# Kernel optimization log

Measured on AMD Instinct MI355X. Metric: run time of the kernel, lower is better.

The kernel has to match this reference:

```python
import jax, jax.numpy as jnp
import numpy as np

B, S, H = 4, 2048, 1024
NH, HD = 16, 64  # num heads, head size

def setup_inputs() -> dict:
    key = jax.random.key(0)
    ks = jax.random.split(key, 7)
    s = 1.0 / np.sqrt(H)
    return {
        "hidden_states": jax.random.normal(ks[0], (B, S, H), dtype=jnp.float32),
        "Wq": jax.random.normal(ks[1], (H, H), dtype=jnp.float32) * s,
        "bq": jax.random.normal(ks[2], (H,), dtype=jnp.float32) * 0.02,
        "Wk": jax.random.normal(ks[3], (H, H), dtype=jnp.float32) * s,
        "bk": jax.random.normal(ks[4], (H,), dtype=jnp.float32) * 0.02,
        "Wv": jax.random.normal(ks[5], (H, H), dtype=jnp.float32) * s,
        "bv": jax.random.normal(ks[6], (H,), dtype=jnp.float32) * 0.02,
    }

def _split_heads(x):
    # [B,S,H] -> [B,NH,S,HD]
    return x.reshape(B, S, NH, HD).transpose(0, 2, 1, 3)

def reference(hidden_states, Wq, bq, Wk, bk, Wv, bv):
    q = _split_heads(hidden_states @ Wq + bq)
    k = _split_heads(hidden_states @ Wk + bk)
    v = _split_heads(hidden_states @ Wv + bv)
    scores = jnp.einsum('bhqd,bhkd->bhqk', q, k) / np.sqrt(HD).astype(np.float32)
    probs = jax.nn.softmax(scores, axis=-1)  # dropout p=0 (eval)
    ctx = jnp.einsum('bhqk,bhkd->bhqd', probs, v)
    # [B,NH,S,HD] -> [B,S,H]
    return ctx.transpose(0, 2, 1, 3).reshape(B, S, H)
```

## Files before the change

### kernel.cpp

```cpp
#include <hip/hip_runtime.h>


typedef __bf16 bf16x8 __attribute__((ext_vector_type(8)));
typedef __bf16 bf16x4 __attribute__((ext_vector_type(4)));
typedef float f32x4 __attribute__((ext_vector_type(4)));
typedef unsigned short ushort8 __attribute__((ext_vector_type(8)));

#define MFMA16(a, b, c) __builtin_amdgcn_mfma_f32_16x16x32_bf16(a, b, c, 0, 0, 0)

static __device__ __forceinline__ unsigned short f2bf(float x) {
    unsigned int u = __float_as_uint(x);
    u = u + 0x7fffu + ((u >> 16) & 1u);
    return (unsigned short)(u >> 16);
}

static __device__ __forceinline__ void gload_lds16(const void* g, void* l) {
    __builtin_amdgcn_global_load_lds(
        (const __attribute__((address_space(1))) unsigned int*)g,
        (__attribute__((address_space(3))) unsigned int*)l,
        16, 0, 0);
}

__global__ void convert_x(const float* __restrict__ x, unsigned short* __restrict__ y) {
    size_t i = ((size_t)blockIdx.x * 256 + threadIdx.x) * 8;
    float4 a = *(const float4*)(x + i);
    float4 b = *(const float4*)(x + i + 4);
    ushort8 o;
    o[0] = f2bf(a.x); o[1] = f2bf(a.y); o[2] = f2bf(a.z); o[3] = f2bf(a.w);
    o[4] = f2bf(b.x); o[5] = f2bf(b.y); o[6] = f2bf(b.z); o[7] = f2bf(b.w);
    *(ushort8*)(y + i) = o;
}

__global__ void wtrans(const float* __restrict__ Wq, const float* __restrict__ Wk,
                       const float* __restrict__ Wv, unsigned short* __restrict__ Wt) {
    __shared__ float T[64][68];
    const float* W = blockIdx.z == 0 ? Wq : (blockIdx.z == 1 ? Wk : Wv);
    int k0 = blockIdx.y * 64, n0 = blockIdx.x * 64;
    int t = threadIdx.x;
    int rr = t >> 2, c4 = (t & 3) * 16;
    for (int j = 0; j < 16; j += 4) {
        float4 v = *(const float4*)(W + (size_t)(k0 + rr) * 1024 + n0 + c4 + j);
        T[rr][c4 + j] = v.x; T[rr][c4 + j + 1] = v.y;
        T[rr][c4 + j + 2] = v.z; T[rr][c4 + j + 3] = v.w;
    }
    __syncthreads();
    unsigned short* o = Wt + ((size_t)blockIdx.z << 20) + (size_t)(n0 + rr) * 1024 + k0 + c4;
    for (int j = 0; j < 16; j += 8) {
        ushort8 v;
        for (int u = 0; u < 8; u++) v[u] = f2bf(T[c4 + j + u][rr]);
        *(ushort8*)(o + j) = v;
    }
}

__global__ __launch_bounds__(256, 2) void qkv_gemm(
    const unsigned short* __restrict__ Xb, const unsigned short* __restrict__ Wt,
    const float* __restrict__ bq, const float* __restrict__ bk, const float* __restrict__ bv,
    unsigned short* __restrict__ Q, unsigned short* __restrict__ K,
    unsigned short* __restrict__ Vt) {
    __shared__ __align__(16) unsigned char smem[65536];

    int tid = threadIdx.x;
    int wave = tid >> 6, lane = tid & 63;
    int g = lane >> 4, r = lane & 15;
    int f = blockIdx.x + blockIdx.y * 24;
    int nf = (f & 7) * 192 + (f >> 3);
    int bx = nf % 24, by = nf / 24;
    int m0 = by * 128;
    int col0 = bx * 128;
    int qkv = col0 >> 10;
    int ncol0 = col0 & 1023;
    int wr = wave >> 1, wc = wave & 1;
    const unsigned short* Wb = Wt + ((size_t)qkv << 20);

    auto stage = [&](int buf, int k0) {
#pragma unroll
        for (int i = 0; i < 4; i++) {
            int slot = (i * 4 + wave) * 64 + lane;
            int row = slot >> 3;
            int ch = (slot & 7) ^ (row & 7);
            gload_lds16(Xb + (size_t)(m0 + row) * 1024 + k0 + ch * 8,
                        smem + buf * 16384 + (i * 4 + wave) * 1024);
            gload_lds16(Wb + (size_t)(ncol0 + row) * 1024 + k0 + ch * 8,
                        smem + 32768 + buf * 16384 + (i * 4 + wave) * 1024);
        }
    };

    f32x4 acc[4][4];
    for (int m = 0; m < 4; m++)
        for (int n = 0; n < 4; n++)
            for (int u = 0; u < 4; u++) acc[m][n][u] = 0.f;

    stage(0, 0);
    __syncthreads();
    int buf = 0;
    for (int t = 0; t < 16; ++t) {
        if (t < 15) stage(buf ^ 1, (t + 1) * 64);
        const unsigned char* Ab = smem + buf * 16384;
        const unsigned char* Bb = smem + 32768 + buf * 16384;
#pragma unroll
        for (int kk = 0; kk < 2; kk++) {
            bf16x8 af[4], bfv[4];
#pragma unroll
            for (int m = 0; m < 4; m++) {
                int row = wr * 64 + m * 16 + r;
                af[m] = *(const bf16x8*)(Ab + row * 128 + ((((kk * 4 + g) << 4)) ^ ((row & 7) << 4)));
            }
#pragma unroll
            for (int n = 0; n < 4; n++) {
                int row = wc * 64 + n * 16 + r;
                bfv[n] = *(const bf16x8*)(Bb + row * 128 + ((((kk * 4 + g) << 4)) ^ ((row & 7) << 4)));
            }
#pragma unroll
            for (int m = 0; m < 4; m++)
#pragma unroll
                for (int n = 0; n < 4; n++)
                    acc[m][n] = MFMA16(af[m], bfv[n], acc[m][n]);
        }
        __syncthreads();
        buf ^= 1;
    }

    if (qkv != 2) {
        const float* bias = (qkv == 0) ? bq : bk;
        unsigned short* dst = (qkv == 0) ? Q : K;
        float scale = (qkv == 0) ? 0.18033688011112042f : 1.0f;
        for (int m = 0; m < 4; m++)
            for (int n = 0; n < 4; n++) {
                int C = ncol0 + wc * 64 + n * 16 + r;
                int h = C >> 6, d = C & 63;
                float bb = bias[C];
                for (int reg = 0; reg < 4; reg++) {
                    int R = m0 + wr * 64 + m * 16 + 4 * g + reg;
                    int b = R >> 11, s = R & 2047;
                    float val = (acc[m][n][reg] + bb) * scale;
                    dst[((((size_t)b * 16 + h) * 2048) + s) * 64 + d] = f2bf(val);
                }
            }
    } else {
        unsigned short* T = (unsigned short*)smem;
        for (int m = 0; m < 4; m++)
            for (int n = 0; n < 4; n++) {
                int Cl = wc * 64 + n * 16 + r;
                float bb = bv[ncol0 + Cl];
                for (int reg = 0; reg < 4; reg++) {
                    int Rl = wr * 64 + m * 16 + 4 * g + reg;
                    T[Rl * 136 + Cl] = f2bf(acc[m][n][reg] + bb);
                }
            }
        __syncthreads();
        int dl = tid >> 1, s0c = (tid & 1) * 64;
        int Cg = ncol0 + dl;
        int h = Cg >> 6, dd = Cg & 63;
        int bidx = m0 >> 11;
        int sbase = (m0 & 2047) + s0c;
        unsigned short* dstp = Vt + (((size_t)bidx * 16 + h) * 64 + dd) * 2048 + sbase;
        for (int jc = 0; jc < 8; jc++) {
            ushort8 v;
            for (int u = 0; u < 8; u++) v[u] = T[(s0c + jc * 8 + u) * 136 + dl];
            *(ushort8*)(dstp + jc * 8) = v;
        }
    }
}

__global__ __launch_bounds__(256, 4) void attn(
    const unsigned short* __restrict__ Q, const unsigned short* __restrict__ K,
    const unsigned short* __restrict__ Vt, float* __restrict__ out) {
    __shared__ __align__(16) unsigned char lds[40960];

    int tid = threadIdx.x, w = tid >> 6, lane = tid & 63;
    int r = lane & 15, g = lane >> 4;
    int f = blockIdx.x + (blockIdx.y << 4);
    int nf = ((f & 7) << 7) | (f >> 3);
    int qt = nf & 15, bh = nf >> 4;
    int q0 = qt * 128 + w * 32;
    const unsigned short* Qb = Q + (size_t)bh * 2048 * 64;
    const unsigned short* Kb = K + (size_t)bh * 2048 * 64;
    const unsigned short* Vb = Vt + (size_t)bh * 64 * 2048;

    auto stageKV = [&](int buf, int kv0) {
#pragma unroll
        for (int i = 0; i < 2; i++) {
            int slot = (i * 4 + w) * 64 + lane;
            int row = slot >> 3;
            int ch = (slot & 7) ^ (row & 7);
            gload_lds16(Kb + (size_t)(kv0 + row) * 64 + ch * 8,
                        lds + buf * 8192 + (i * 4 + w) * 1024);
            gload_lds16(Vb + (size_t)row * 2048 + kv0 + ch * 8,
                        lds + 16384 + buf * 8192 + (i * 4 + w) * 1024);
        }
    };

    bf16x8 qf[2][2];
#pragma unroll
    for (int qi = 0; qi < 2; qi++)
#pragma unroll
        for (int sl = 0; sl < 2; sl++)
            qf[qi][sl] = *(const bf16x8*)(Qb + (size_t)(q0 + qi * 16 + r) * 64 + sl * 32 + g * 8);

    bf16x8 ones8;
#pragma unroll
    for (int i = 0; i < 8; i++) ones8[i] = (__bf16)1.0f;

    f32x4 o[2][4], ls[2];
#pragma unroll
    for (int qi = 0; qi < 2; qi++) {
#pragma unroll
        for (int u = 0; u < 4; u++) ls[qi][u] = 0.f;
#pragma unroll
        for (int d = 0; d < 4; d++)
#pragma unroll
            for (int u = 0; u < 4; u++) o[qi][d][u] = 0.f;
    }

    stageKV(0, 0);
    __syncthreads();
    int buf = 0;
    int rsw = (r & 7) << 4;
    unsigned char* Pw = lds + 32768 + w * 2048;

    for (int t = 0; t < 32; ++t) {
        if (t < 31) stageKV(buf ^ 1, (t + 1) * 64);
        const unsigned char* Kl = lds + buf * 8192;
        const unsigned char* Vl = lds + 16384 + buf * 8192;

        f32x4 s[2][4];
#pragma unroll
        for (int qi = 0; qi < 2; qi++)
#pragma unroll
            for (int kvt = 0; kvt < 4; kvt++)
#pragma unroll
                for (int u = 0; u < 4; u++) s[qi][kvt][u] = 0.f;
#pragma unroll
        for (int kvt = 0; kvt < 4; kvt++) {
            const unsigned char* kp = Kl + (kvt * 16 + r) * 128;
            bf16x8 k0 = *(const bf16x8*)(kp + ((g << 4) ^ rsw));
            bf16x8 k1 = *(const bf16x8*)(kp + (((4 + g) << 4) ^ rsw));
            s[0][kvt] = MFMA16(k0, qf[0][0], s[0][kvt]);
            s[0][kvt] = MFMA16(k1, qf[0][1], s[0][kvt]);
            s[1][kvt] = MFMA16(k0, qf[1][0], s[1][kvt]);
            s[1][kvt] = MFMA16(k1, qf[1][1], s[1][kvt]);
        }

#pragma unroll
        for (int qi = 0; qi < 2; qi++) {
#pragma unroll
            for (int kvt = 0; kvt < 4; kvt++) {
                bf16x4 pw;
                pw[0] = (__bf16)__builtin_amdgcn_exp2f(s[qi][kvt][0]);
                pw[1] = (__bf16)__builtin_amdgcn_exp2f(s[qi][kvt][1]);
                pw[2] = (__bf16)__builtin_amdgcn_exp2f(s[qi][kvt][2]);
                pw[3] = (__bf16)__builtin_amdgcn_exp2f(s[qi][kvt][3]);
                *(bf16x4*)(Pw + (r << 7) + ((kvt * 32 + g * 8) ^ rsw)) = pw;
            }
#pragma unroll
            for (int ks2 = 0; ks2 < 2; ks2++) {
                bf16x8 pf = *(const bf16x8*)(Pw + (r << 7) + ((ks2 * 64 + g * 16) ^ rsw));
                ls[qi] = MFMA16(ones8, pf, ls[qi]);
#pragma unroll
                for (int d = 0; d < 4; d++) {
                    bf16x8 vf = *(const bf16x8*)(Vl + (d * 16 + r) * 128 + (((ks2 * 4 + g) << 4) ^ rsw));
                    o[qi][d] = MFMA16(vf, pf, o[qi][d]);
                }
            }
        }

        __syncthreads();
        buf ^= 1;
    }

    int b = bh >> 4, h = bh & 15;
#pragma unroll
    for (int qi = 0; qi < 2; qi++) {
        float inv = 1.0f / ls[qi][0];
        float* ob = out + ((size_t)b * 2048 + q0 + qi * 16 + r) * 1024 + h * 64;
#pragma unroll
        for (int d = 0; d < 4; d++) {
            float4 v;
            v.x = o[qi][d][0] * inv; v.y = o[qi][d][1] * inv;
            v.z = o[qi][d][2] * inv; v.w = o[qi][d][3] * inv;
            *(float4*)(ob + d * 16 + 4 * g) = v;
        }
    }
}

extern "C" void kernel_launch(void* const* d_in, const int* in_sizes, int n_in,
                              void* d_out, int out_size, void* d_ws, size_t ws_size,
                              hipStream_t stream) {
    const float* X  = (const float*)d_in[0];
    const float* Wq = (const float*)d_in[1];
    const float* bq = (const float*)d_in[2];
    const float* Wk = (const float*)d_in[3];
    const float* bk = (const float*)d_in[4];
    const float* Wv = (const float*)d_in[5];
    const float* bv = (const float*)d_in[6];
    float* out = (float*)d_out;
    char* ws = (char*)d_ws;

    unsigned short* Xb  = (unsigned short*)(ws);
    unsigned short* Wt  = (unsigned short*)(ws + 16777216);
    unsigned short* Qw  = (unsigned short*)(ws + 23068672);
    unsigned short* Kw  = (unsigned short*)(ws + 39845888);
    unsigned short* Vtw = (unsigned short*)(ws + 56623104);

    hipLaunchKernelGGL(convert_x, dim3(4096), dim3(256), 0, stream, X, Xb);
    hipLaunchKernelGGL(wtrans, dim3(16, 16, 3), dim3(256), 0, stream, Wq, Wk, Wv, Wt);
    hipLaunchKernelGGL(qkv_gemm, dim3(24, 64), dim3(256), 0, stream,
                       Xb, Wt, bq, bk, bv, Qw, Kw, Vtw);
    hipLaunchKernelGGL(attn, dim3(16, 64), dim3(256), 0, stream, Qw, Kw, Vtw, out);
}
```

Baseline: 157.0 us.

## Software-pipeline attention loop: overlap next QK with previous softmax-PV using triple-buffered V

```diff
diff --git a/kernel.cpp b/kernel.cpp
--- a/kernel.cpp
+++ b/kernel.cpp
@@ -162,10 +162,10 @@
     }
 }
 
-__global__ __launch_bounds__(256, 4) void attn(
+__global__ __launch_bounds__(256, 2) void attn(
     const unsigned short* __restrict__ Q, const unsigned short* __restrict__ K,
     const unsigned short* __restrict__ Vt, float* __restrict__ out) {
-    __shared__ __align__(16) unsigned char lds[40960];
+    __shared__ __align__(16) unsigned char lds[49152];
 
     int tid = threadIdx.x, w = tid >> 6, lane = tid & 63;
     int r = lane & 15, g = lane >> 4;
@@ -177,16 +177,16 @@
     const unsigned short* Kb = K + (size_t)bh * 2048 * 64;
     const unsigned short* Vb = Vt + (size_t)bh * 64 * 2048;
 
-    auto stageKV = [&](int buf, int kv0) {
+    auto stageKV = [&](int kbuf, int vbuf, int kv0) {
 #pragma unroll
         for (int i = 0; i < 2; i++) {
             int slot = (i * 4 + w) * 64 + lane;
             int row = slot >> 3;
             int ch = (slot & 7) ^ (row & 7);
             gload_lds16(Kb + (size_t)(kv0 + row) * 64 + ch * 8,
-                        lds + buf * 8192 + (i * 4 + w) * 1024);
+                        lds + kbuf * 8192 + (i * 4 + w) * 1024);
             gload_lds16(Vb + (size_t)row * 2048 + kv0 + ch * 8,
-                        lds + 16384 + buf * 8192 + (i * 4 + w) * 1024);
+                        lds + 16384 + vbuf * 8192 + (i * 4 + w) * 1024);
         }
     };
 
@@ -212,61 +212,79 @@
             for (int u = 0; u < 4; u++) o[qi][d][u] = 0.f;
     }
 
-    stageKV(0, 0);
+    f32x4 sA[2][4], sB[2][4];
+    int rsw = (r & 7) << 4;
+    unsigned char* Pw = lds + 40960 + w * 2048;
+
+#define ZERO_S(S) { \
+    _Pragma("unroll") for (int qz = 0; qz < 2; qz++) \
+    _Pragma("unroll") for (int kz = 0; kz < 4; kz++) \
+    _Pragma("unroll") for (int uz = 0; uz < 4; uz++) S[qz][kz][uz] = 0.f; }
+
+#define QK_PASS(SCUR, KR) { \
+    const unsigned char* Kl_ = lds + (KR) * 8192; \
+    __builtin_amdgcn_s_setprio(1); \
+    _Pragma("unroll") for (int kvt = 0; kvt < 4; kvt++) { \
+        const unsigned char* kp_ = Kl_ + (kvt * 16 + r) * 128; \
+        bf16x8 k0_ = *(const bf16x8*)(kp_ + ((g << 4) ^ rsw)); \
+        bf16x8 k1_ = *(const bf16x8*)(kp_ + (((4 + g) << 4) ^ rsw)); \
+        SCUR[0][kvt] = MFMA16(k0_, qf[0][0], SCUR[0][kvt]); \
+        SCUR[0][kvt] = MFMA16(k1_, qf[0][1], SCUR[0][kvt]); \
+        SCUR[1][kvt] = MFMA16(k0_, qf[1][0], SCUR[1][kvt]); \
+        SCUR[1][kvt] = MFMA16(k1_, qf[1][1], SCUR[1][kvt]); \
+    } \
+    __builtin_amdgcn_s_setprio(0); }
+
+#define SM_PV(SPREV, VPREV) { \
+    const unsigned char* Vl_ = lds + 16384 + (VPREV) * 8192; \
+    _Pragma("unroll") for (int qi = 0; qi < 2; qi++) { \
+        _Pragma("unroll") for (int kvt = 0; kvt < 4; kvt++) { \
+            bf16x4 pw_; \
+            pw_[0] = (__bf16)__builtin_amdgcn_exp2f(SPREV[qi][kvt][0]); \
+            pw_[1] = (__bf16)__builtin_amdgcn_exp2f(SPREV[qi][kvt][1]); \
+            pw_[2] = (__bf16)__builtin_amdgcn_exp2f(SPREV[qi][kvt][2]); \
+            pw_[3] = (__bf16)__builtin_amdgcn_exp2f(SPREV[qi][kvt][3]); \
+            *(bf16x4*)(Pw + (r << 7) + ((kvt * 32 + g * 8) ^ rsw)) = pw_; \
+        } \
+        __builtin_amdgcn_s_setprio(1); \
+        _Pragma("unroll") for (int ks2 = 0; ks2 < 2; ks2++) { \
+            bf16x8 pf_ = *(const bf16x8*)(Pw + (r << 7) + ((ks2 * 64 + g * 16) ^ rsw)); \
+            ls[qi] = MFMA16(ones8, pf_, ls[qi]); \
+            _Pragma("unroll") for (int d = 0; d < 4; d++) { \
+                bf16x8 vf_ = *(const bf16x8*)(Vl_ + (d * 16 + r) * 128 + (((ks2 * 4 + g) << 4) ^ rsw)); \
+                o[qi][d] = MFMA16(vf_, pf_, o[qi][d]); \
+            } \
+        } \
+        __builtin_amdgcn_s_setprio(0); \
+    } }
+
+#define BODY(TT, SCUR, SPREV, KR, KW, VW, VPREV) { \
+    stageKV((KW), (VW), ((TT) + 1) * 64); \
+    ZERO_S(SCUR); \
+    QK_PASS(SCUR, (KR)); \
+    SM_PV(SPREV, (VPREV)); \
+    __syncthreads(); }
+
+    stageKV(0, 0, 0);
     __syncthreads();
-    int buf = 0;
-    int rsw = (r & 7) << 4;
-    unsigned char* Pw = lds + 32768 + w * 2048;
-
-    for (int t = 0; t < 32; ++t) {
-        if (t < 31) stageKV(buf ^ 1, (t + 1) * 64);
-        const unsigned char* Kl = lds + buf * 8192;
-        const unsigned char* Vl = lds + 16384 + buf * 8192;
-
-        f32x4 s[2][4];
-#pragma unroll
-        for (int qi = 0; qi < 2; qi++)
-#pragma unroll
-            for (int kvt = 0; kvt < 4; kvt++)
-#pragma unroll
-                for (int u = 0; u < 4; u++) s[qi][kvt][u] = 0.f;
-#pragma unroll
-        for (int kvt = 0; kvt < 4; kvt++) {
-            const unsigned char* kp = Kl + (kvt * 16 + r) * 128;
-            bf16x8 k0 = *(const bf16x8*)(kp + ((g << 4) ^ rsw));
-            bf16x8 k1 = *(const bf16x8*)(kp + (((4 + g) << 4) ^ rsw));
-            s[0][kvt] = MFMA16(k0, qf[0][0], s[0][kvt]);
-            s[0][kvt] = MFMA16(k1, qf[0][1], s[0][kvt]);
-            s[1][kvt] = MFMA16(k0, qf[1][0], s[1][kvt]);
-            s[1][kvt] = MFMA16(k1, qf[1][1], s[1][kvt]);
-        }
-
-#pragma unroll
-        for (int qi = 0; qi < 2; qi++) {
-#pragma unroll
-            for (int kvt = 0; kvt < 4; kvt++) {
-                bf16x4 pw;
-                pw[0] = (__bf16)__builtin_amdgcn_exp2f(s[qi][kvt][0]);
-                pw[1] = (__bf16)__builtin_amdgcn_exp2f(s[qi][kvt][1]);
-                pw[2] = (__bf16)__builtin_amdgcn_exp2f(s[qi][kvt][2]);
-                pw[3] = (__bf16)__builtin_amdgcn_exp2f(s[qi][kvt][3]);
-                *(bf16x4*)(Pw + (r << 7) + ((kvt * 32 + g * 8) ^ rsw)) = pw;
-            }
-#pragma unroll
-            for (int ks2 = 0; ks2 < 2; ks2++) {
-                bf16x8 pf = *(const bf16x8*)(Pw + (r << 7) + ((ks2 * 64 + g * 16) ^ rsw));
-                ls[qi] = MFMA16(ones8, pf, ls[qi]);
-#pragma unroll
-                for (int d = 0; d < 4; d++) {
-                    bf16x8 vf = *(const bf16x8*)(Vl + (d * 16 + r) * 128 + (((ks2 * 4 + g) << 4) ^ rsw));
-                    o[qi][d] = MFMA16(vf, pf, o[qi][d]);
-                }
-            }
-        }
-
-        __syncthreads();
-        buf ^= 1;
-    }
+    stageKV(1, 1, 64);
+    ZERO_S(sA);
+    QK_PASS(sA, 0);
+    __syncthreads();
+
+    for (int base = 1; base <= 25; base += 6) {
+        BODY(base + 0, sB, sA, 1, 0, 2, 0);
+        BODY(base + 1, sA, sB, 0, 1, 0, 1);
+        BODY(base + 2, sB, sA, 1, 0, 1, 2);
+        BODY(base + 3, sA, sB, 0, 1, 2, 0);
+        BODY(base + 4, sB, sA, 1, 0, 0, 1);
+        BODY(base + 5, sA, sB, 0, 1, 1, 2);
+    }
+
+    ZERO_S(sB);
+    QK_PASS(sB, 1);
+    SM_PV(sA, 0);
+    SM_PV(sB, 1);
 
     int b = bh >> 4, h = bh & 15;
 #pragma unroll
@@ -281,6 +299,10 @@
             *(float4*)(ob + d * 16 + 4 * g) = v;
         }
     }
+#undef BODY
+#undef SM_PV
+#undef QK_PASS
+#undef ZERO_S
 }
 
 extern "C" void kernel_launch(void* const* d_in, const int* in_sizes, int n_in,
```

After: 167.5 us. 1.07x slower.
